# Optimization experiments

Hardware: AMD Instinct MI355X
Metric: run time of the kernel (lower is better)

## Reference

```python
import jax, jax.numpy as jnp
import numpy as np

BS, N, FEAT = 4, 4096, 64
LN_EPS = 1e-5


def setup_inputs() -> dict:
    key = jax.random.key(0)
    k1, k2, k3 = jax.random.split(key, 3)
    positions = jax.random.normal(k1, (BS, N, 3), dtype=jnp.float32)
    # nn.Linear(n_point, feature_dim): weight (FEAT, N), bias (FEAT,)
    W = jax.random.normal(k2, (FEAT, N), dtype=jnp.float32) * (1.0 / np.sqrt(N))
    b = jax.random.normal(k3, (FEAT,), dtype=jnp.float32) * 0.02
    gamma = jnp.ones((FEAT,), dtype=jnp.float32)
    beta = jnp.zeros((FEAT,), dtype=jnp.float32)
    return {"positions": positions, "W": W, "b": b, "gamma": gamma, "beta": beta}


def reference(positions, W, b, gamma, beta):
    # all-pairs squared distances: (bs, N, N)
    diff = positions[:, :, None, :] - positions[:, None, :, :]  # (bs,N,N,3)
    sq = jnp.sum(diff * diff, axis=-1)                          # (bs,N,N)
    # safe sqrt (diagonal is exactly 0)
    safe = jnp.where(sq > 0, sq, 1.0)
    dist = jnp.where(sq > 0, jnp.sqrt(safe), 0.0)               # (bs,N,N)
    # Linear(N -> FEAT)
    x = jnp.einsum('bnm,fm->bnf', dist, W) + b                  # (bs,N,FEAT)
    # LayerNorm over last dim (biased variance, eps=1e-5)
    mu = jnp.mean(x, axis=-1, keepdims=True)
    var = jnp.mean((x - mu) ** 2, axis=-1, keepdims=True)
    xn = (x - mu) / jnp.sqrt(var + LN_EPS) * gamma + beta
    # SiLU
    return xn * jax.nn.sigmoid(xn)
```

## Files before the change

### kernel.cpp

```cpp
#include <hip/hip_runtime.h>


typedef float f32x4 __attribute__((ext_vector_type(4)));
typedef __bf16 bf16x8 __attribute__((ext_vector_type(8)));

union BF8 { bf16x8 v; uint4 u; };

#define N_PTS 4096
#define FEATD 64
#define BK 256
#define NCH (N_PTS / BK)

__global__ void wconv_kernel(const float* __restrict__ W,
                             unsigned short* __restrict__ Wbt) {
  int gid = blockIdx.x * blockDim.x + threadIdx.x;
  int f = gid >> 9, m8 = gid & 511;
  const float4* src = (const float4*)(W + (size_t)f * N_PTS + m8 * 8);
  float4 a = src[0], b = src[1];
  BF8 o;
  o.v[0] = (__bf16)a.x; o.v[1] = (__bf16)a.y; o.v[2] = (__bf16)a.z; o.v[3] = (__bf16)a.w;
  o.v[4] = (__bf16)b.x; o.v[5] = (__bf16)b.y; o.v[6] = (__bf16)b.z; o.v[7] = (__bf16)b.w;
  ((uint4*)Wbt)[(size_t)m8 * 64 + f] = o.u;
}

__device__ __forceinline__ void load_lds16(const void* g, void* l) {
  __builtin_amdgcn_global_load_lds(
      (const __attribute__((address_space(1))) void*)g,
      (__attribute__((address_space(3))) void*)l, 16, 0, 0);
}

__global__ __launch_bounds__(1024, 4) void frp_kernel(
    const float* __restrict__ pos, const float* __restrict__ W,
    const float* __restrict__ bias, const float* __restrict__ gamma,
    const float* __restrict__ beta, const unsigned short* __restrict__ Wbt,
    float* __restrict__ out) {
  __shared__ uint4 Wbuf[2][2048];
  __shared__ __align__(16) float Px[N_PTS];
  __shared__ __align__(16) float Py[N_PTS];
  __shared__ __align__(16) float Pz[N_PTS];

  const int tid = threadIdx.x;
  const int lane = tid & 63;
  const int wave = tid >> 6;
  const int rs  = wave & 1;
  const int ksl = wave >> 1;
  const int fx = lane & 15;
  const int q = lane >> 4;

  const int batch = blockIdx.x >> 6;
  const int nb = (blockIdx.x & 63) * 64;
  const float* posB = pos + (size_t)batch * N_PTS * 3;

  {
    const float4* p4 = (const float4*)posB;
    float4 f0 = p4[tid * 3 + 0];
    float4 f1 = p4[tid * 3 + 1];
    float4 f2 = p4[tid * 3 + 2];
    ((float4*)Px)[tid] = make_float4(f0.x, f0.w, f1.z, f2.y);
    ((float4*)Py)[tid] = make_float4(f0.y, f1.x, f1.w, f2.z);
    ((float4*)Pz)[tid] = make_float4(f0.z, f1.y, f2.x, f2.w);
  }

  const bool useWb = (Wbt != nullptr);

  auto stageW = [&](int c, int b) {
#pragma unroll
    for (int it = 0; it < 2; ++it) {
      int gi = it * 1024 + tid;
      if (useWb) {
        load_lds16(Wbt + ((size_t)c * 2048 + gi) * 8, &Wbuf[b][gi]);
      } else {
        int g = gi >> 6, f = gi & 63;
        const float4* src = (const float4*)(W + (size_t)f * N_PTS + c * BK + g * 8);
        float4 a = src[0], b2 = src[1];
        BF8 o;
        o.v[0] = (__bf16)a.x;  o.v[1] = (__bf16)a.y;  o.v[2] = (__bf16)a.z;  o.v[3] = (__bf16)a.w;
        o.v[4] = (__bf16)b2.x; o.v[5] = (__bf16)b2.y; o.v[6] = (__bf16)b2.z; o.v[7] = (__bf16)b2.w;
        Wbuf[b][gi] = o.u;
      }
    }
  };

  f32x4 acc[2][4];
#pragma unroll
  for (int a = 0; a < 2; ++a)
#pragma unroll
    for (int t = 0; t < 4; ++t) acc[a][t] = (f32x4){0.f, 0.f, 0.f, 0.f};

  stageW(0, 0);
  __syncthreads();

  const int nrow0 = nb + rs * 32 + fx;
  const float px0 = Px[nrow0],      py0 = Py[nrow0],      pz0 = Pz[nrow0];
  const float px1 = Px[nrow0 + 16], py1 = Py[nrow0 + 16], pz1 = Pz[nrow0 + 16];

  const int g8 = ksl * 4 + q;

  for (int c = 0; c < NCH; ++c) {
    if (c + 1 < NCH) stageW(c + 1, (c + 1) & 1);
    const uint4* Wcur = Wbuf[c & 1];
    const int m4 = c * 64 + g8 * 2;
    f32x4 xa = ((const f32x4*)Px)[m4], xb = ((const f32x4*)Px)[m4 + 1];
    f32x4 ya = ((const f32x4*)Py)[m4], yb = ((const f32x4*)Py)[m4 + 1];
    f32x4 za = ((const f32x4*)Pz)[m4], zb = ((const f32x4*)Pz)[m4 + 1];

    bf16x8 af0, af1;
    {
      f32x4 dx = xa - px0, dy = ya - py0, dz = za - pz0;
      f32x4 sq = dx * dx + dy * dy + dz * dz;
#pragma unroll
      for (int j = 0; j < 4; ++j) af0[j] = (__bf16)__builtin_amdgcn_sqrtf(sq[j]);
      dx = xb - px0; dy = yb - py0; dz = zb - pz0;
      sq = dx * dx + dy * dy + dz * dz;
#pragma unroll
      for (int j = 0; j < 4; ++j) af0[4 + j] = (__bf16)__builtin_amdgcn_sqrtf(sq[j]);
      dx = xa - px1; dy = ya - py1; dz = za - pz1;
      sq = dx * dx + dy * dy + dz * dz;
#pragma unroll
      for (int j = 0; j < 4; ++j) af1[j] = (__bf16)__builtin_amdgcn_sqrtf(sq[j]);
      dx = xb - px1; dy = yb - py1; dz = zb - pz1;
      sq = dx * dx + dy * dy + dz * dz;
#pragma unroll
      for (int j = 0; j < 4; ++j) af1[4 + j] = (__bf16)__builtin_amdgcn_sqrtf(sq[j]);
    }
#pragma unroll
    for (int t = 0; t < 4; ++t) {
      BF8 bw;
      bw.u = Wcur[g8 * 64 + t * 16 + fx];
      acc[0][t] = __builtin_amdgcn_mfma_f32_16x16x32_bf16(af0, bw.v, acc[0][t], 0, 0, 0);
      acc[1][t] = __builtin_amdgcn_mfma_f32_16x16x32_bf16(af1, bw.v, acc[1][t], 0, 0, 0);
    }
    __syncthreads();
  }

  f32x4* mbv = (f32x4*)Wbuf;
  __syncthreads();
  if (ksl >= 4) {
    int w = (ksl - 4) * 2 + rs;
#pragma unroll
    for (int a = 0; a < 2; ++a)
#pragma unroll
      for (int t = 0; t < 4; ++t)
        mbv[w * 512 + (a * 4 + t) * 64 + lane] = acc[a][t];
  }
  __syncthreads();
  if (ksl < 4) {
    int w = ksl * 2 + rs;
#pragma unroll
    for (int a = 0; a < 2; ++a)
#pragma unroll
      for (int t = 0; t < 4; ++t)
        acc[a][t] += mbv[w * 512 + (a * 4 + t) * 64 + lane];
  }
  __syncthreads();
  if (ksl >= 1 && ksl < 4) {
    int w = (ksl - 1) * 2 + rs;
#pragma unroll
    for (int a = 0; a < 2; ++a)
#pragma unroll
      for (int t = 0; t < 4; ++t)
        mbv[w * 512 + (a * 4 + t) * 64 + lane] = acc[a][t];
  }
  __syncthreads();
  if (ksl == 0) {
#pragma unroll
    for (int s = 0; s < 3; ++s)
#pragma unroll
      for (int a = 0; a < 2; ++a)
#pragma unroll
        for (int t = 0; t < 4; ++t)
          acc[a][t] += mbv[(s * 2 + rs) * 512 + (a * 4 + t) * 64 + lane];

    float bb[4], gg[4], be[4];
#pragma unroll
    for (int t = 0; t < 4; ++t) {
      bb[t] = bias[t * 16 + fx];
      gg[t] = gamma[t * 16 + fx];
      be[t] = beta[t * 16 + fx];
    }
    float* outB = out + ((size_t)batch * N_PTS + nb + rs * 32) * FEATD;
#pragma unroll
    for (int a = 0; a < 2; ++a) {
#pragma unroll
      for (int r = 0; r < 4; ++r) {
        float x[4], d[4];
#pragma unroll
        for (int t = 0; t < 4; ++t) x[t] = acc[a][t][r] + bb[t];
        float s = x[0] + x[1] + x[2] + x[3];
        s += __shfl_xor(s, 1); s += __shfl_xor(s, 2);
        s += __shfl_xor(s, 4); s += __shfl_xor(s, 8);
        float mu = s * (1.f / 64.f);
        float v = 0.f;
#pragma unroll
        for (int t = 0; t < 4; ++t) { d[t] = x[t] - mu; v += d[t] * d[t]; }
        v += __shfl_xor(v, 1); v += __shfl_xor(v, 2);
        v += __shfl_xor(v, 4); v += __shfl_xor(v, 8);
        float rstd = __builtin_amdgcn_rsqf(v * (1.f / 64.f) + 1e-5f);
        float* orow = outB + (a * 16 + q * 4 + r) * FEATD;
#pragma unroll
        for (int t = 0; t < 4; ++t) {
          float xn = d[t] * rstd * gg[t] + be[t];
          float y = xn * (1.f / (1.f + __expf(-xn)));
          orow[t * 16 + fx] = y;
        }
      }
    }
  }
}

extern "C" void kernel_launch(void* const* d_in, const int* in_sizes, int n_in,
                              void* d_out, int out_size, void* d_ws, size_t ws_size,
                              hipStream_t stream) {
  const float* pos   = (const float*)d_in[0];
  const float* W     = (const float*)d_in[1];
  const float* bias  = (const float*)d_in[2];
  const float* gamma = (const float*)d_in[3];
  const float* beta  = (const float*)d_in[4];
  float* out = (float*)d_out;

  const size_t wb_bytes = (size_t)FEATD * N_PTS * sizeof(unsigned short);
  int use_ws = (d_ws != nullptr && ws_size >= wb_bytes);
  unsigned short* Wbt = use_ws ? (unsigned short*)d_ws : nullptr;

  if (use_ws) {
    wconv_kernel<<<dim3((FEATD * N_PTS / 8) / 256), dim3(256), 0, stream>>>(W, Wbt);
  }
  frp_kernel<<<dim3(256), dim3(1024), 0, stream>>>(pos, W, bias, gamma, beta, Wbt, out);
}
```

Measured before the change: 86.86 us.

## Give each wave a private W slice and drop per-chunk block barriers

Halves the block to 512 threads. Each wave now computes all 64 output rows for its own K-slice and double-buffers that slice of bf16 W in a wave-private LDS region. Completion is tracked with explicit `s_waitcnt vmcnt` instead of a `__syncthreads` every chunk. This is meant to remove block-wide barrier stalls and to reuse each loaded W fragment across four MFMA row tiles. The cost is more accumulator registers per thread, fewer waves per block for latency hiding, and a reworked multi-step LDS reduction across waves.

```diff
diff --git a/kernel.cpp b/kernel.cpp
--- a/kernel.cpp
+++ b/kernel.cpp
@@ -29,12 +29,12 @@
       (__attribute__((address_space(3))) void*)l, 16, 0, 0);
 }
 
-__global__ __launch_bounds__(1024, 4) void frp_kernel(
+__global__ __launch_bounds__(512, 2) void frp_kernel(
     const float* __restrict__ pos, const float* __restrict__ W,
     const float* __restrict__ bias, const float* __restrict__ gamma,
     const float* __restrict__ beta, const unsigned short* __restrict__ Wbt,
     float* __restrict__ out) {
-  __shared__ uint4 Wbuf[2][2048];
+  __shared__ uint4 Wall[2][8][256];
   __shared__ __align__(16) float Px[N_PTS];
   __shared__ __align__(16) float Py[N_PTS];
   __shared__ __align__(16) float Pz[N_PTS];
@@ -42,8 +42,6 @@
   const int tid = threadIdx.x;
   const int lane = tid & 63;
   const int wave = tid >> 6;
-  const int rs  = wave & 1;
-  const int ksl = wave >> 1;
   const int fx = lane & 15;
   const int q = lane >> 4;
 
@@ -53,123 +51,154 @@
 
   {
     const float4* p4 = (const float4*)posB;
-    float4 f0 = p4[tid * 3 + 0];
-    float4 f1 = p4[tid * 3 + 1];
-    float4 f2 = p4[tid * 3 + 2];
-    ((float4*)Px)[tid] = make_float4(f0.x, f0.w, f1.z, f2.y);
-    ((float4*)Py)[tid] = make_float4(f0.y, f1.x, f1.w, f2.z);
-    ((float4*)Pz)[tid] = make_float4(f0.z, f1.y, f2.x, f2.w);
+    float4 f0 = p4[tid * 6 + 0], f1 = p4[tid * 6 + 1], f2 = p4[tid * 6 + 2];
+    float4 f3 = p4[tid * 6 + 3], f4 = p4[tid * 6 + 4], f5 = p4[tid * 6 + 5];
+    ((float4*)Px)[tid * 2 + 0] = make_float4(f0.x, f0.w, f1.z, f2.y);
+    ((float4*)Px)[tid * 2 + 1] = make_float4(f3.x, f3.w, f4.z, f5.y);
+    ((float4*)Py)[tid * 2 + 0] = make_float4(f0.y, f1.x, f1.w, f2.z);
+    ((float4*)Py)[tid * 2 + 1] = make_float4(f3.y, f4.x, f4.w, f5.z);
+    ((float4*)Pz)[tid * 2 + 0] = make_float4(f0.z, f1.y, f2.x, f2.w);
+    ((float4*)Pz)[tid * 2 + 1] = make_float4(f3.z, f4.y, f5.x, f5.w);
   }
 
   const bool useWb = (Wbt != nullptr);
 
-  auto stageW = [&](int c, int b) {
-#pragma unroll
-    for (int it = 0; it < 2; ++it) {
-      int gi = it * 1024 + tid;
-      if (useWb) {
-        load_lds16(Wbt + ((size_t)c * 2048 + gi) * 8, &Wbuf[b][gi]);
-      } else {
-        int g = gi >> 6, f = gi & 63;
-        const float4* src = (const float4*)(W + (size_t)f * N_PTS + c * BK + g * 8);
-        float4 a = src[0], b2 = src[1];
+  if (useWb) {
+#pragma unroll
+    for (int i = 0; i < 4; ++i)
+      load_lds16(Wbt + ((size_t)((wave * 4 + i) * 64 + lane)) * 8,
+                 &Wall[0][wave][i * 64 + lane]);
+  }
+
+  f32x4 acc[4][4];
+#pragma unroll
+  for (int a = 0; a < 4; ++a)
+#pragma unroll
+    for (int t = 0; t < 4; ++t) acc[a][t] = (f32x4){0.f, 0.f, 0.f, 0.f};
+
+  if (useWb) asm volatile("s_waitcnt vmcnt(0)" ::: "memory");
+  __syncthreads();
+
+  float pxr[4], pyr[4], pzr[4];
+#pragma unroll
+  for (int a = 0; a < 4; ++a) {
+    int r = nb + a * 16 + fx;
+    pxr[a] = Px[r]; pyr[a] = Py[r]; pzr[a] = Pz[r];
+  }
+
+  const f32x4* Px4 = (const f32x4*)Px;
+  const f32x4* Py4 = (const f32x4*)Py;
+  const f32x4* Pz4 = (const f32x4*)Pz;
+
+#pragma unroll 2
+  for (int c = 0; c < NCH; ++c) {
+    if (useWb) {
+      const int cn = (c + 1) & (NCH - 1);
+      const int bufn = (c + 1) & 1;
+#pragma unroll
+      for (int i = 0; i < 4; ++i)
+        load_lds16(Wbt + ((size_t)((cn * 32 + wave * 4 + i) * 64 + lane)) * 8,
+                   &Wall[bufn][wave][i * 64 + lane]);
+    } else {
+#pragma unroll
+      for (int i = 0; i < 4; ++i) {
+        const float4* src =
+            (const float4*)(W + (size_t)lane * N_PTS + c * BK + (wave * 4 + i) * 8);
+        float4 a4 = src[0], b4 = src[1];
         BF8 o;
-        o.v[0] = (__bf16)a.x;  o.v[1] = (__bf16)a.y;  o.v[2] = (__bf16)a.z;  o.v[3] = (__bf16)a.w;
-        o.v[4] = (__bf16)b2.x; o.v[5] = (__bf16)b2.y; o.v[6] = (__bf16)b2.z; o.v[7] = (__bf16)b2.w;
-        Wbuf[b][gi] = o.u;
+        o.v[0] = (__bf16)a4.x; o.v[1] = (__bf16)a4.y; o.v[2] = (__bf16)a4.z; o.v[3] = (__bf16)a4.w;
+        o.v[4] = (__bf16)b4.x; o.v[5] = (__bf16)b4.y; o.v[6] = (__bf16)b4.z; o.v[7] = (__bf16)b4.w;
+        Wall[0][wave][i * 64 + lane] = o.u;
       }
     }
-  };
-
-  f32x4 acc[2][4];
-#pragma unroll
-  for (int a = 0; a < 2; ++a)
-#pragma unroll
-    for (int t = 0; t < 4; ++t) acc[a][t] = (f32x4){0.f, 0.f, 0.f, 0.f};
-
-  stageW(0, 0);
-  __syncthreads();
-
-  const int nrow0 = nb + rs * 32 + fx;
-  const float px0 = Px[nrow0],      py0 = Py[nrow0],      pz0 = Pz[nrow0];
-  const float px1 = Px[nrow0 + 16], py1 = Py[nrow0 + 16], pz1 = Pz[nrow0 + 16];
-
-  const int g8 = ksl * 4 + q;
-
-  for (int c = 0; c < NCH; ++c) {
-    if (c + 1 < NCH) stageW(c + 1, (c + 1) & 1);
-    const uint4* Wcur = Wbuf[c & 1];
-    const int m4 = c * 64 + g8 * 2;
-    f32x4 xa = ((const f32x4*)Px)[m4], xb = ((const f32x4*)Px)[m4 + 1];
-    f32x4 ya = ((const f32x4*)Py)[m4], yb = ((const f32x4*)Py)[m4 + 1];
-    f32x4 za = ((const f32x4*)Pz)[m4], zb = ((const f32x4*)Pz)[m4 + 1];
-
-    bf16x8 af0, af1;
-    {
-      f32x4 dx = xa - px0, dy = ya - py0, dz = za - pz0;
+
+    const int m4 = c * 64 + (wave * 4 + q) * 2;
+    f32x4 xa = Px4[m4], xb = Px4[m4 + 1];
+    f32x4 ya = Py4[m4], yb = Py4[m4 + 1];
+    f32x4 za = Pz4[m4], zb = Pz4[m4 + 1];
+
+    bf16x8 af[4];
+#pragma unroll
+    for (int a = 0; a < 4; ++a) {
+      f32x4 dx = xa - pxr[a], dy = ya - pyr[a], dz = za - pzr[a];
       f32x4 sq = dx * dx + dy * dy + dz * dz;
 #pragma unroll
-      for (int j = 0; j < 4; ++j) af0[j] = (__bf16)__builtin_amdgcn_sqrtf(sq[j]);
-      dx = xb - px0; dy = yb - py0; dz = zb - pz0;
+      for (int j = 0; j < 4; ++j) af[a][j] = (__bf16)__builtin_amdgcn_sqrtf(sq[j]);
+      dx = xb - pxr[a]; dy = yb - pyr[a]; dz = zb - pzr[a];
       sq = dx * dx + dy * dy + dz * dz;
 #pragma unroll
-      for (int j = 0; j < 4; ++j) af0[4 + j] = (__bf16)__builtin_amdgcn_sqrtf(sq[j]);
-      dx = xa - px1; dy = ya - py1; dz = za - pz1;
-      sq = dx * dx + dy * dy + dz * dz;
-#pragma unroll
-      for (int j = 0; j < 4; ++j) af1[j] = (__bf16)__builtin_amdgcn_sqrtf(sq[j]);
-      dx = xb - px1; dy = yb - py1; dz = zb - pz1;
-      sq = dx * dx + dy * dy + dz * dz;
-#pragma unroll
-      for (int j = 0; j < 4; ++j) af1[4 + j] = (__bf16)__builtin_amdgcn_sqrtf(sq[j]);
-    }
+      for (int j = 0; j < 4; ++j) af[a][4 + j] = (__bf16)__builtin_amdgcn_sqrtf(sq[j]);
+    }
+
+    if (useWb) {
+      asm volatile("s_waitcnt vmcnt(4)" ::: "memory");
+    }
+
+    const uint4* Wl = &Wall[useWb ? (c & 1) : 0][wave][0];
 #pragma unroll
     for (int t = 0; t < 4; ++t) {
       BF8 bw;
-      bw.u = Wcur[g8 * 64 + t * 16 + fx];
-      acc[0][t] = __builtin_amdgcn_mfma_f32_16x16x32_bf16(af0, bw.v, acc[0][t], 0, 0, 0);
-      acc[1][t] = __builtin_amdgcn_mfma_f32_16x16x32_bf16(af1, bw.v, acc[1][t], 0, 0, 0);
-    }
-    __syncthreads();
-  }
-
-  f32x4* mbv = (f32x4*)Wbuf;
-  __syncthreads();
-  if (ksl >= 4) {
-    int w = (ksl - 4) * 2 + rs;
-#pragma unroll
-    for (int a = 0; a < 2; ++a)
-#pragma unroll
-      for (int t = 0; t < 4; ++t)
-        mbv[w * 512 + (a * 4 + t) * 64 + lane] = acc[a][t];
-  }
-  __syncthreads();
-  if (ksl < 4) {
-    int w = ksl * 2 + rs;
-#pragma unroll
-    for (int a = 0; a < 2; ++a)
-#pragma unroll
-      for (int t = 0; t < 4; ++t)
-        acc[a][t] += mbv[w * 512 + (a * 4 + t) * 64 + lane];
-  }
-  __syncthreads();
-  if (ksl >= 1 && ksl < 4) {
-    int w = (ksl - 1) * 2 + rs;
-#pragma unroll
-    for (int a = 0; a < 2; ++a)
-#pragma unroll
-      for (int t = 0; t < 4; ++t)
-        mbv[w * 512 + (a * 4 + t) * 64 + lane] = acc[a][t];
-  }
-  __syncthreads();
-  if (ksl == 0) {
-#pragma unroll
-    for (int s = 0; s < 3; ++s)
-#pragma unroll
-      for (int a = 0; a < 2; ++a)
-#pragma unroll
-        for (int t = 0; t < 4; ++t)
-          acc[a][t] += mbv[(s * 2 + rs) * 512 + (a * 4 + t) * 64 + lane];
+      bw.u = Wl[q * 64 + t * 16 + fx];
+#pragma unroll
+      for (int a = 0; a < 4; ++a)
+        acc[a][t] = __builtin_amdgcn_mfma_f32_16x16x32_bf16(af[a], bw.v, acc[a][t], 0, 0, 0);
+    }
+  }
+
+  f32x4* mbv = (f32x4*)Wall;
+  if (useWb) asm volatile("s_waitcnt vmcnt(0)" ::: "memory");
+  __syncthreads();
+  if (wave >= 4) {
+#pragma unroll
+    for (int a = 0; a < 4; ++a)
+#pragma unroll
+      for (int t = 0; t < 4; ++t)
+        mbv[(wave - 4) * 1024 + (a * 4 + t) * 64 + lane] = acc[a][t];
+  }
+  __syncthreads();
+  if (wave < 4) {
+#pragma unroll
+    for (int a = 0; a < 4; ++a)
+#pragma unroll
+      for (int t = 0; t < 4; ++t)
+        acc[a][t] += mbv[wave * 1024 + (a * 4 + t) * 64 + lane];
+  }
+  __syncthreads();
+  if (wave == 2 || wave == 3) {
+#pragma unroll
+    for (int a = 0; a < 4; ++a)
+#pragma unroll
+      for (int t = 0; t < 4; ++t)
+        mbv[(wave - 2) * 1024 + (a * 4 + t) * 64 + lane] = acc[a][t];
+  }
+  __syncthreads();
+  if (wave < 2) {
+#pragma unroll
+    for (int a = 0; a < 4; ++a)
+#pragma unroll
+      for (int t = 0; t < 4; ++t)
+        acc[a][t] += mbv[wave * 1024 + (a * 4 + t) * 64 + lane];
+  }
+  __syncthreads();
+  if (wave < 2) {
+#pragma unroll
+    for (int ai = 0; ai < 2; ++ai) {
+      const int a = (wave == 0) ? (2 + ai) : ai;
+#pragma unroll
+      for (int t = 0; t < 4; ++t)
+        mbv[(2 + wave) * 1024 + (ai * 4 + t) * 64 + lane] = acc[a][t];
+    }
+  }
+  __syncthreads();
+  if (wave < 2) {
+    const int src = (wave == 0) ? 3 : 2;
+#pragma unroll
+    for (int ai = 0; ai < 2; ++ai) {
+      const int a = wave * 2 + ai;
+#pragma unroll
+      for (int t = 0; t < 4; ++t)
+        acc[a][t] += mbv[src * 1024 + (ai * 4 + t) * 64 + lane];
+    }
 
     float bb[4], gg[4], be[4];
 #pragma unroll
@@ -178,9 +207,10 @@
       gg[t] = gamma[t * 16 + fx];
       be[t] = beta[t * 16 + fx];
     }
-    float* outB = out + ((size_t)batch * N_PTS + nb + rs * 32) * FEATD;
-#pragma unroll
-    for (int a = 0; a < 2; ++a) {
+    float* outB = out + ((size_t)batch * N_PTS + nb) * FEATD;
+#pragma unroll
+    for (int ai = 0; ai < 2; ++ai) {
+      const int a = wave * 2 + ai;
 #pragma unroll
       for (int r = 0; r < 4; ++r) {
         float x[4], d[4];
@@ -225,5 +255,5 @@
   if (use_ws) {
     wconv_kernel<<<dim3((FEATD * N_PTS / 8) / 256), dim3(256), 0, stream>>>(W, Wbt);
   }
-  frp_kernel<<<dim3(256), dim3(1024), 0, stream>>>(pos, W, bias, gamma, beta, Wbt, out);
-}
+  frp_kernel<<<dim3(256), dim3(512), 0, stream>>>(pos, W, bias, gamma, beta, Wbt, out);
+}
```

After: 113.4 us. 30.5% more time.

## Load positions and weights directly from global memory into registers, dropping LDS staging

Applied to the files above, without the earlier changes.

The main loop no longer double-buffers bf16 weight chunks into LDS or copies all positions into LDS. Each wave reads its own K-slice of position and weight data straight from global memory (likely L2-resident) into registers, which removes the per-chunk __syncthreads barriers. Shared memory shrinks to just the reduction buffer, and the cross-wave reduction becomes a binary tree with more barriers but fewer reads per step. The cost is more global and L2 traffic and load latency with no LDS reuse across waves, plus redundant position loads across blocks.

```diff
diff --git a/kernel.cpp b/kernel.cpp
--- a/kernel.cpp
+++ b/kernel.cpp
@@ -8,8 +8,6 @@
 
 #define N_PTS 4096
 #define FEATD 64
-#define BK 256
-#define NCH (N_PTS / BK)
 
 __global__ void wconv_kernel(const float* __restrict__ W,
                              unsigned short* __restrict__ Wbt) {
@@ -23,21 +21,12 @@
   ((uint4*)Wbt)[(size_t)m8 * 64 + f] = o.u;
 }
 
-__device__ __forceinline__ void load_lds16(const void* g, void* l) {
-  __builtin_amdgcn_global_load_lds(
-      (const __attribute__((address_space(1))) void*)g,
-      (__attribute__((address_space(3))) void*)l, 16, 0, 0);
-}
-
 __global__ __launch_bounds__(1024, 4) void frp_kernel(
     const float* __restrict__ pos, const float* __restrict__ W,
     const float* __restrict__ bias, const float* __restrict__ gamma,
     const float* __restrict__ beta, const unsigned short* __restrict__ Wbt,
     float* __restrict__ out) {
-  __shared__ uint4 Wbuf[2][2048];
-  __shared__ __align__(16) float Px[N_PTS];
-  __shared__ __align__(16) float Py[N_PTS];
-  __shared__ __align__(16) float Pz[N_PTS];
+  __shared__ f32x4 mbv[4096];
 
   const int tid = threadIdx.x;
   const int lane = tid & 63;
@@ -50,91 +39,79 @@
   const int batch = blockIdx.x >> 6;
   const int nb = (blockIdx.x & 63) * 64;
   const float* posB = pos + (size_t)batch * N_PTS * 3;
-
-  {
-    const float4* p4 = (const float4*)posB;
-    float4 f0 = p4[tid * 3 + 0];
-    float4 f1 = p4[tid * 3 + 1];
-    float4 f2 = p4[tid * 3 + 2];
-    ((float4*)Px)[tid] = make_float4(f0.x, f0.w, f1.z, f2.y);
-    ((float4*)Py)[tid] = make_float4(f0.y, f1.x, f1.w, f2.z);
-    ((float4*)Pz)[tid] = make_float4(f0.z, f1.y, f2.x, f2.w);
-  }
-
+  const float4* p4 = (const float4*)posB;
+
+  float pxr[2], pyr[2], pzr[2];
+#pragma unroll
+  for (int a = 0; a < 2; ++a) {
+    int r = nb + rs * 32 + a * 16 + fx;
+    pxr[a] = posB[r * 3 + 0];
+    pyr[a] = posB[r * 3 + 1];
+    pzr[a] = posB[r * 3 + 2];
+  }
+
+  f32x4 acc[2][4];
+#pragma unroll
+  for (int a = 0; a < 2; ++a)
+#pragma unroll
+    for (int t = 0; t < 4; ++t) acc[a][t] = (f32x4){0.f, 0.f, 0.f, 0.f};
+
+  const uint4* Wg = (const uint4*)Wbt;
   const bool useWb = (Wbt != nullptr);
 
-  auto stageW = [&](int c, int b) {
-#pragma unroll
-    for (int it = 0; it < 2; ++it) {
-      int gi = it * 1024 + tid;
-      if (useWb) {
-        load_lds16(Wbt + ((size_t)c * 2048 + gi) * 8, &Wbuf[b][gi]);
-      } else {
-        int g = gi >> 6, f = gi & 63;
-        const float4* src = (const float4*)(W + (size_t)f * N_PTS + c * BK + g * 8);
-        float4 a = src[0], b2 = src[1];
+#pragma unroll 2
+  for (int s = 0; s < 16; ++s) {
+    const int G = ksl * 64 + s * 4 + q;
+
+    float4 f0 = p4[G * 6 + 0], f1 = p4[G * 6 + 1], f2 = p4[G * 6 + 2];
+    float4 f3 = p4[G * 6 + 3], f4 = p4[G * 6 + 4], f5 = p4[G * 6 + 5];
+
+    uint4 bw[4];
+    if (useWb) {
+#pragma unroll
+      for (int t = 0; t < 4; ++t) bw[t] = Wg[G * 64 + t * 16 + fx];
+    } else {
+#pragma unroll
+      for (int t = 0; t < 4; ++t) {
+        const float4* src = (const float4*)(W + (size_t)(t * 16 + fx) * N_PTS + G * 8);
+        float4 a4 = src[0], b4 = src[1];
         BF8 o;
-        o.v[0] = (__bf16)a.x;  o.v[1] = (__bf16)a.y;  o.v[2] = (__bf16)a.z;  o.v[3] = (__bf16)a.w;
-        o.v[4] = (__bf16)b2.x; o.v[5] = (__bf16)b2.y; o.v[6] = (__bf16)b2.z; o.v[7] = (__bf16)b2.w;
-        Wbuf[b][gi] = o.u;
+        o.v[0] = (__bf16)a4.x; o.v[1] = (__bf16)a4.y; o.v[2] = (__bf16)a4.z; o.v[3] = (__bf16)a4.w;
+        o.v[4] = (__bf16)b4.x; o.v[5] = (__bf16)b4.y; o.v[6] = (__bf16)b4.z; o.v[7] = (__bf16)b4.w;
+        bw[t] = o.u;
       }
     }
-  };
-
-  f32x4 acc[2][4];
-#pragma unroll
-  for (int a = 0; a < 2; ++a)
-#pragma unroll
-    for (int t = 0; t < 4; ++t) acc[a][t] = (f32x4){0.f, 0.f, 0.f, 0.f};
-
-  stageW(0, 0);
-  __syncthreads();
-
-  const int nrow0 = nb + rs * 32 + fx;
-  const float px0 = Px[nrow0],      py0 = Py[nrow0],      pz0 = Pz[nrow0];
-  const float px1 = Px[nrow0 + 16], py1 = Py[nrow0 + 16], pz1 = Pz[nrow0 + 16];
-
-  const int g8 = ksl * 4 + q;
-
-  for (int c = 0; c < NCH; ++c) {
-    if (c + 1 < NCH) stageW(c + 1, (c + 1) & 1);
-    const uint4* Wcur = Wbuf[c & 1];
-    const int m4 = c * 64 + g8 * 2;
-    f32x4 xa = ((const f32x4*)Px)[m4], xb = ((const f32x4*)Px)[m4 + 1];
-    f32x4 ya = ((const f32x4*)Py)[m4], yb = ((const f32x4*)Py)[m4 + 1];
-    f32x4 za = ((const f32x4*)Pz)[m4], zb = ((const f32x4*)Pz)[m4 + 1];
-
-    bf16x8 af0, af1;
-    {
-      f32x4 dx = xa - px0, dy = ya - py0, dz = za - pz0;
+
+    f32x4 xa = (f32x4){f0.x, f0.w, f1.z, f2.y};
+    f32x4 xb = (f32x4){f3.x, f3.w, f4.z, f5.y};
+    f32x4 ya = (f32x4){f0.y, f1.x, f1.w, f2.z};
+    f32x4 yb = (f32x4){f3.y, f4.x, f4.w, f5.z};
+    f32x4 za = (f32x4){f0.z, f1.y, f2.x, f2.w};
+    f32x4 zb = (f32x4){f3.z, f4.y, f5.x, f5.w};
+
+    bf16x8 af[2];
+#pragma unroll
+    for (int a = 0; a < 2; ++a) {
+      f32x4 dx = xa - pxr[a], dy = ya - pyr[a], dz = za - pzr[a];
       f32x4 sq = dx * dx + dy * dy + dz * dz;
 #pragma unroll
-      for (int j = 0; j < 4; ++j) af0[j] = (__bf16)__builtin_amdgcn_sqrtf(sq[j]);
-      dx = xb - px0; dy = yb - py0; dz = zb - pz0;
+      for (int j = 0; j < 4; ++j) af[a][j] = (__bf16)__builtin_amdgcn_sqrtf(sq[j]);
+      dx = xb - pxr[a]; dy = yb - pyr[a]; dz = zb - pzr[a];
       sq = dx * dx + dy * dy + dz * dz;
 #pragma unroll
-      for (int j = 0; j < 4; ++j) af0[4 + j] = (__bf16)__builtin_amdgcn_sqrtf(sq[j]);
-      dx = xa - px1; dy = ya - py1; dz = za - pz1;
-      sq = dx * dx + dy * dy + dz * dz;
-#pragma unroll
-      for (int j = 0; j < 4; ++j) af1[j] = (__bf16)__builtin_amdgcn_sqrtf(sq[j]);
-      dx = xb - px1; dy = yb - py1; dz = zb - pz1;
-      sq = dx * dx + dy * dy + dz * dz;
-#pragma unroll
-      for (int j = 0; j < 4; ++j) af1[4 + j] = (__bf16)__builtin_amdgcn_sqrtf(sq[j]);
-    }
+      for (int j = 0; j < 4; ++j) af[a][4 + j] = (__bf16)__builtin_amdgcn_sqrtf(sq[j]);
+    }
+
 #pragma unroll
     for (int t = 0; t < 4; ++t) {
-      BF8 bw;
-      bw.u = Wcur[g8 * 64 + t * 16 + fx];
-      acc[0][t] = __builtin_amdgcn_mfma_f32_16x16x32_bf16(af0, bw.v, acc[0][t], 0, 0, 0);
-      acc[1][t] = __builtin_amdgcn_mfma_f32_16x16x32_bf16(af1, bw.v, acc[1][t], 0, 0, 0);
-    }
-    __syncthreads();
-  }
-
-  f32x4* mbv = (f32x4*)Wbuf;
-  __syncthreads();
+      BF8 bwv;
+      bwv.u = bw[t];
+#pragma unroll
+      for (int a = 0; a < 2; ++a)
+        acc[a][t] = __builtin_amdgcn_mfma_f32_16x16x32_bf16(af[a], bwv.v, acc[a][t], 0, 0, 0);
+    }
+  }
+
   if (ksl >= 4) {
     int w = (ksl - 4) * 2 + rs;
 #pragma unroll
@@ -153,8 +130,8 @@
         acc[a][t] += mbv[w * 512 + (a * 4 + t) * 64 + lane];
   }
   __syncthreads();
-  if (ksl >= 1 && ksl < 4) {
-    int w = (ksl - 1) * 2 + rs;
+  if (ksl == 2 || ksl == 3) {
+    int w = (ksl - 2) * 2 + rs;
 #pragma unroll
     for (int a = 0; a < 2; ++a)
 #pragma unroll
@@ -162,14 +139,29 @@
         mbv[w * 512 + (a * 4 + t) * 64 + lane] = acc[a][t];
   }
   __syncthreads();
+  if (ksl < 2) {
+    int w = ksl * 2 + rs;
+#pragma unroll
+    for (int a = 0; a < 2; ++a)
+#pragma unroll
+      for (int t = 0; t < 4; ++t)
+        acc[a][t] += mbv[w * 512 + (a * 4 + t) * 64 + lane];
+  }
+  __syncthreads();
+  if (ksl == 1) {
+#pragma unroll
+    for (int a = 0; a < 2; ++a)
+#pragma unroll
+      for (int t = 0; t < 4; ++t)
+        mbv[rs * 512 + (a * 4 + t) * 64 + lane] = acc[a][t];
+  }
+  __syncthreads();
   if (ksl == 0) {
 #pragma unroll
-    for (int s = 0; s < 3; ++s)
-#pragma unroll
-      for (int a = 0; a < 2; ++a)
-#pragma unroll
-        for (int t = 0; t < 4; ++t)
-          acc[a][t] += mbv[(s * 2 + rs) * 512 + (a * 4 + t) * 64 + lane];
+    for (int a = 0; a < 2; ++a)
+#pragma unroll
+      for (int t = 0; t < 4; ++t)
+        acc[a][t] += mbv[rs * 512 + (a * 4 + t) * 64 + lane];
 
     float bb[4], gg[4], be[4];
 #pragma unroll
```

Result: slower. 91.27 us (+5.1%).

## Use per-wave private LDS staging and register-prefetched positions to drop block barriers

Applied to the files above, without the earlier changes.

Removes the shared Px/Py/Pz LDS arrays and instead has each wave prefetch its position chunk straight from global memory into registers one iteration ahead. Weight tiles are staged into per-wave private LDS double buffers via global_load_lds, synchronised with explicit vmcnt waits, so the per-chunk __syncthreads is gone. The goal is to cut block-wide barrier stalls and let waves run independently. The cost is duplicated global reads of W across the waves that share a k-slice, and correctness now rests on hand-written vmcnt counts.

```diff
diff --git a/kernel.cpp b/kernel.cpp
--- a/kernel.cpp
+++ b/kernel.cpp
@@ -34,10 +34,7 @@
     const float* __restrict__ bias, const float* __restrict__ gamma,
     const float* __restrict__ beta, const unsigned short* __restrict__ Wbt,
     float* __restrict__ out) {
-  __shared__ uint4 Wbuf[2][2048];
-  __shared__ __align__(16) float Px[N_PTS];
-  __shared__ __align__(16) float Py[N_PTS];
-  __shared__ __align__(16) float Pz[N_PTS];
+  __shared__ uint4 Wpriv[2][16][256];
 
   const int tid = threadIdx.x;
   const int lane = tid & 63;
@@ -50,59 +47,52 @@
   const int batch = blockIdx.x >> 6;
   const int nb = (blockIdx.x & 63) * 64;
   const float* posB = pos + (size_t)batch * N_PTS * 3;
-
+  const float4* p4 = (const float4*)posB;
+
+  const int nrow0 = nb + rs * 32 + fx;
+  const float px0 = posB[nrow0 * 3 + 0],        py0 = posB[nrow0 * 3 + 1],        pz0 = posB[nrow0 * 3 + 2];
+  const float px1 = posB[(nrow0 + 16) * 3 + 0], py1 = posB[(nrow0 + 16) * 3 + 1], pz1 = posB[(nrow0 + 16) * 3 + 2];
+
+  const bool useWb = (Wbt != nullptr);
+  const int g8 = ksl * 4 + q;
+
+  auto stageW = [&](int c, int b) {
+#pragma unroll
+    for (int i = 0; i < 4; ++i)
+      load_lds16(Wbt + ((size_t)(c * 2048 + (ksl * 4 + i) * 64 + lane)) * 8,
+                 &Wpriv[b][wave][i * 64 + lane]);
+  };
+
+  f32x4 acc[2][4];
+#pragma unroll
+  for (int a = 0; a < 2; ++a)
+#pragma unroll
+    for (int t = 0; t < 4; ++t) acc[a][t] = (f32x4){0.f, 0.f, 0.f, 0.f};
+
+  float4 f0, f1, f2, f3, f4, f5;
   {
-    const float4* p4 = (const float4*)posB;
-    float4 f0 = p4[tid * 3 + 0];
-    float4 f1 = p4[tid * 3 + 1];
-    float4 f2 = p4[tid * 3 + 2];
-    ((float4*)Px)[tid] = make_float4(f0.x, f0.w, f1.z, f2.y);
-    ((float4*)Py)[tid] = make_float4(f0.y, f1.x, f1.w, f2.z);
-    ((float4*)Pz)[tid] = make_float4(f0.z, f1.y, f2.x, f2.w);
-  }
-
-  const bool useWb = (Wbt != nullptr);
-
-  auto stageW = [&](int c, int b) {
-#pragma unroll
-    for (int it = 0; it < 2; ++it) {
-      int gi = it * 1024 + tid;
-      if (useWb) {
-        load_lds16(Wbt + ((size_t)c * 2048 + gi) * 8, &Wbuf[b][gi]);
-      } else {
-        int g = gi >> 6, f = gi & 63;
-        const float4* src = (const float4*)(W + (size_t)f * N_PTS + c * BK + g * 8);
-        float4 a = src[0], b2 = src[1];
-        BF8 o;
-        o.v[0] = (__bf16)a.x;  o.v[1] = (__bf16)a.y;  o.v[2] = (__bf16)a.z;  o.v[3] = (__bf16)a.w;
-        o.v[4] = (__bf16)b2.x; o.v[5] = (__bf16)b2.y; o.v[6] = (__bf16)b2.z; o.v[7] = (__bf16)b2.w;
-        Wbuf[b][gi] = o.u;
-      }
-    }
-  };
-
-  f32x4 acc[2][4];
-#pragma unroll
-  for (int a = 0; a < 2; ++a)
-#pragma unroll
-    for (int t = 0; t < 4; ++t) acc[a][t] = (f32x4){0.f, 0.f, 0.f, 0.f};
-
-  stageW(0, 0);
-  __syncthreads();
-
-  const int nrow0 = nb + rs * 32 + fx;
-  const float px0 = Px[nrow0],      py0 = Py[nrow0],      pz0 = Pz[nrow0];
-  const float px1 = Px[nrow0 + 16], py1 = Py[nrow0 + 16], pz1 = Pz[nrow0 + 16];
-
-  const int g8 = ksl * 4 + q;
-
+    const int G = g8;
+    f0 = p4[G * 6 + 0]; f1 = p4[G * 6 + 1]; f2 = p4[G * 6 + 2];
+    f3 = p4[G * 6 + 3]; f4 = p4[G * 6 + 4]; f5 = p4[G * 6 + 5];
+  }
+  if (useWb) stageW(0, 0);
+
+#pragma unroll 2
   for (int c = 0; c < NCH; ++c) {
-    if (c + 1 < NCH) stageW(c + 1, (c + 1) & 1);
-    const uint4* Wcur = Wbuf[c & 1];
-    const int m4 = c * 64 + g8 * 2;
-    f32x4 xa = ((const f32x4*)Px)[m4], xb = ((const f32x4*)Px)[m4 + 1];
-    f32x4 ya = ((const f32x4*)Py)[m4], yb = ((const f32x4*)Py)[m4 + 1];
-    f32x4 za = ((const f32x4*)Pz)[m4], zb = ((const f32x4*)Pz)[m4 + 1];
+    float4 n0, n1, n2, n3, n4, n5;
+    if (c + 1 < NCH) {
+      const int Gn = (c + 1) * 32 + g8;
+      n0 = p4[Gn * 6 + 0]; n1 = p4[Gn * 6 + 1]; n2 = p4[Gn * 6 + 2];
+      n3 = p4[Gn * 6 + 3]; n4 = p4[Gn * 6 + 4]; n5 = p4[Gn * 6 + 5];
+    }
+    __builtin_amdgcn_sched_barrier(0);
+
+    f32x4 xa = (f32x4){f0.x, f0.w, f1.z, f2.y};
+    f32x4 xb = (f32x4){f3.x, f3.w, f4.z, f5.y};
+    f32x4 ya = (f32x4){f0.y, f1.x, f1.w, f2.z};
+    f32x4 yb = (f32x4){f3.y, f4.x, f4.w, f5.z};
+    f32x4 za = (f32x4){f0.z, f1.y, f2.x, f2.w};
+    f32x4 zb = (f32x4){f3.z, f4.y, f5.x, f5.w};
 
     bf16x8 af0, af1;
     {
@@ -123,17 +113,39 @@
 #pragma unroll
       for (int j = 0; j < 4; ++j) af1[4 + j] = (__bf16)__builtin_amdgcn_sqrtf(sq[j]);
     }
-#pragma unroll
-    for (int t = 0; t < 4; ++t) {
-      BF8 bw;
-      bw.u = Wcur[g8 * 64 + t * 16 + fx];
-      acc[0][t] = __builtin_amdgcn_mfma_f32_16x16x32_bf16(af0, bw.v, acc[0][t], 0, 0, 0);
-      acc[1][t] = __builtin_amdgcn_mfma_f32_16x16x32_bf16(af1, bw.v, acc[1][t], 0, 0, 0);
-    }
-    __syncthreads();
-  }
-
-  f32x4* mbv = (f32x4*)Wbuf;
+
+    if (useWb) {
+      if (c < NCH - 1) asm volatile("s_waitcnt vmcnt(6)" ::: "memory");
+      else             asm volatile("s_waitcnt vmcnt(0)" ::: "memory");
+      __builtin_amdgcn_sched_barrier(0);
+
+      const uint4* Wl = &Wpriv[c & 1][wave][0];
+#pragma unroll
+      for (int t = 0; t < 4; ++t) {
+        BF8 bw;
+        bw.u = Wl[q * 64 + t * 16 + fx];
+        acc[0][t] = __builtin_amdgcn_mfma_f32_16x16x32_bf16(af0, bw.v, acc[0][t], 0, 0, 0);
+        acc[1][t] = __builtin_amdgcn_mfma_f32_16x16x32_bf16(af1, bw.v, acc[1][t], 0, 0, 0);
+      }
+      if (c + 1 < NCH) stageW(c + 1, (c + 1) & 1);
+    } else {
+#pragma unroll
+      for (int t = 0; t < 4; ++t) {
+        const int G = c * 32 + g8;
+        const float4* src = (const float4*)(W + (size_t)(t * 16 + fx) * N_PTS + G * 8);
+        float4 a4 = src[0], b4 = src[1];
+        BF8 bw;
+        bw.v[0] = (__bf16)a4.x; bw.v[1] = (__bf16)a4.y; bw.v[2] = (__bf16)a4.z; bw.v[3] = (__bf16)a4.w;
+        bw.v[4] = (__bf16)b4.x; bw.v[5] = (__bf16)b4.y; bw.v[6] = (__bf16)b4.z; bw.v[7] = (__bf16)b4.w;
+        acc[0][t] = __builtin_amdgcn_mfma_f32_16x16x32_bf16(af0, bw.v, acc[0][t], 0, 0, 0);
+        acc[1][t] = __builtin_amdgcn_mfma_f32_16x16x32_bf16(af1, bw.v, acc[1][t], 0, 0, 0);
+      }
+    }
+
+    if (c + 1 < NCH) { f0 = n0; f1 = n1; f2 = n2; f3 = n3; f4 = n4; f5 = n5; }
+  }
+
+  f32x4* mbv = (f32x4*)Wpriv;
   __syncthreads();
   if (ksl >= 4) {
     int w = (ksl - 4) * 2 + rs;
```

Result: slower. 156.1 us (+79.7%).
